# Kernel tuning notes

Measured on AMD Instinct MI355X. Metric: run time of the kernel, lower is better.

The kernel has to match this reference:

```python
import math
import jax, jax.numpy as jnp
import numpy as np

N_HEADS = 16

def setup_inputs() -> dict:
    key = jax.random.key(0)
    k1, k2, k3 = jax.random.split(key, 3)
    B, S, D = 2, 2048, 1024
    x = jax.random.normal(k1, (B, S, D), dtype=jnp.float32)
    W_qkv = jax.random.normal(k2, (3 * D, D), dtype=jnp.float32)
    W_o = jax.random.normal(k3, (D, D), dtype=jnp.float32)
    return {"x": x, "W_qkv": W_qkv, "W_o": W_o}


def reference(x, W_qkv, W_o):
    B, S, D = x.shape
    H = N_HEADS
    d_h = D // H
    # fused QKV projection: (B,S,3D)
    t = jnp.matmul(x, W_qkv.T)
    t = t.reshape(B, S, 3, D)
    # NOTE: module reshapes (B,S,D) -> (B,H,S,d_h) directly (no transpose);
    # heads partition the flattened seq*feature layout. Replicate exactly.
    q = t[:, :, 0, :].reshape(B, H, S, d_h)
    k = t[:, :, 1, :].reshape(B, H, S, d_h)
    v = t[:, :, 2, :].reshape(B, H, S, d_h)
    # scaled by sqrt(d_model), as in the original (not sqrt(d_h))
    scores = jnp.einsum('bhqd,bhkd->bhqk', q, k) / math.sqrt(D)
    scores = jnp.tril(scores)
    # original sets ALL exact zeros to -inf (masks upper triangle)
    scores = jnp.where(scores == 0, -jnp.inf, scores)
    attn = jax.nn.softmax(scores, axis=-1)
    y_prime = jnp.matmul(attn, v)  # (B,H,S,d_h)
    y_prime = y_prime.transpose(0, 2, 1, 3).reshape(B, S, D)
    y = jnp.matmul(y_prime, W_o.T)
    return y
```

## Files before the change

kernel.cpp:

```cpp
#include <hip/hip_runtime.h>
#include <hip/hip_bf16.h>


using bf16 = __hip_bfloat16;
typedef __attribute__((ext_vector_type(8))) short bf16x8v;
typedef __attribute__((ext_vector_type(4))) float f32x4;

#define MFMA_BF16(A, B, C) __builtin_amdgcn_mfma_f32_16x16x32_bf16((A), (B), (C), 0, 0, 0)

#define GLD_LDS16(g, l)                                                        \
  __builtin_amdgcn_global_load_lds(                                            \
      (const __attribute__((address_space(1))) void*)(g),                      \
      (__attribute__((address_space(3))) void*)(l), 16, 0, 0)

static __device__ __forceinline__ unsigned short bf_bits(float f) {
  bf16 b = __float2bfloat16(f);
  return *reinterpret_cast<unsigned short*>(&b);
}

__global__ __launch_bounds__(256) void cvt_split(const float* __restrict__ in,
                                                 bf16* __restrict__ hi,
                                                 bf16* __restrict__ lo, int n) {
  int i = (blockIdx.x * 256 + threadIdx.x) * 4;
  if (i >= n) return;
  const float4 v = *(const float4*)(in + i);
  float vv[4] = {v.x, v.y, v.z, v.w};
  ushort4 hb, lb;
  unsigned short* hp = &hb.x;
  unsigned short* lp = &lb.x;
#pragma unroll
  for (int j = 0; j < 4; ++j) {
    bf16 h = __float2bfloat16(vv[j]);
    float r = vv[j] - __bfloat162float(h);
    hp[j] = bf_bits(vv[j]);
    lp[j] = bf_bits(r);
  }
  *(ushort4*)(hi + i) = hb;
  *(ushort4*)(lo + i) = lb;
}

__global__ __launch_bounds__(256) void cvt_plain(const float* __restrict__ in,
                                                 bf16* __restrict__ out, int n) {
  int i = (blockIdx.x * 256 + threadIdx.x) * 4;
  if (i >= n) return;
  const float4 v = *(const float4*)(in + i);
  ushort4 ob;
  ob.x = bf_bits(v.x); ob.y = bf_bits(v.y); ob.z = bf_bits(v.z); ob.w = bf_bits(v.w);
  *(ushort4*)(out + i) = ob;
}

__global__ __launch_bounds__(256) void gemm_qkv(
    const bf16* __restrict__ Ah, const bf16* __restrict__ Al,
    const bf16* __restrict__ Bh, const bf16* __restrict__ Bl,
    bf16* __restrict__ Qhi, bf16* __restrict__ Qlo,
    bf16* __restrict__ Khi, bf16* __restrict__ Klo,
    bf16* __restrict__ Vt) {
  const int K = 1024;
  const int NT = 24;
  __shared__ __attribute__((aligned(16))) bf16 AsH[4096], AsL[4096], BsH[4096], BsL[4096];
  const int t = threadIdx.x;
  const int lane = t & 63;
  const int wave = t >> 6;
  const int wr = wave >> 1, wc = wave & 1;
  int bid = blockIdx.x;
  bid = (bid & 7) * (768 >> 3) + (bid >> 3);
  const int bm = bid / NT, bn = bid % NT;
  const int brow = bm * 128, bcol = bn * 128;
  const bool isV = (bcol >= 2048);
  const bf16* pAh = Ah + (size_t)brow * K;
  const bf16* pAl = Al + (size_t)brow * K;
  const bf16* pBh = Bh + (size_t)bcol * K;
  const bf16* pBl = Bl + (size_t)bcol * K;
  const int r0 = t >> 2;
  const int c0 = (t & 3) * 8;
  f32x4 acc[4][4] = {};
  for (int k0 = 0; k0 < K; k0 += 32) {
    __syncthreads();
    GLD_LDS16(pAh + (size_t)r0 * K + k0 + c0,        &AsH[t * 8]);
    GLD_LDS16(pAh + (size_t)(r0 + 64) * K + k0 + c0, &AsH[2048 + t * 8]);
    GLD_LDS16(pBh + (size_t)r0 * K + k0 + c0,        &BsH[t * 8]);
    GLD_LDS16(pBh + (size_t)(r0 + 64) * K + k0 + c0, &BsH[2048 + t * 8]);
    if (!isV) {
      GLD_LDS16(pAl + (size_t)r0 * K + k0 + c0,        &AsL[t * 8]);
      GLD_LDS16(pAl + (size_t)(r0 + 64) * K + k0 + c0, &AsL[2048 + t * 8]);
      GLD_LDS16(pBl + (size_t)r0 * K + k0 + c0,        &BsL[t * 8]);
      GLD_LDS16(pBl + (size_t)(r0 + 64) * K + k0 + c0, &BsL[2048 + t * 8]);
    }
    __syncthreads();
    const int ao = (wr * 64 + (lane & 15)) * 32 + (lane >> 4) * 8;
    const int bo = (wc * 64 + (lane & 15)) * 32 + (lane >> 4) * 8;
    bf16x8v ah[4], bh_[4];
#pragma unroll
    for (int i = 0; i < 4; ++i) {
      ah[i]  = *(const bf16x8v*)&AsH[ao + i * 512];
      bh_[i] = *(const bf16x8v*)&BsH[bo + i * 512];
    }
    if (!isV) {
      bf16x8v al[4], bl_[4];
#pragma unroll
      for (int i = 0; i < 4; ++i) {
        al[i]  = *(const bf16x8v*)&AsL[ao + i * 512];
        bl_[i] = *(const bf16x8v*)&BsL[bo + i * 512];
      }
#pragma unroll
      for (int i = 0; i < 4; ++i)
#pragma unroll
        for (int j = 0; j < 4; ++j) {
          acc[i][j] = MFMA_BF16(ah[i], bh_[j], acc[i][j]);
          acc[i][j] = MFMA_BF16(ah[i], bl_[j], acc[i][j]);
          acc[i][j] = MFMA_BF16(al[i], bh_[j], acc[i][j]);
        }
    } else {
#pragma unroll
      for (int i = 0; i < 4; ++i)
#pragma unroll
        for (int j = 0; j < 4; ++j)
          acc[i][j] = MFMA_BF16(ah[i], bh_[j], acc[i][j]);
    }
  }
#pragma unroll
  for (int i = 0; i < 4; ++i)
#pragma unroll
    for (int j = 0; j < 4; ++j)
#pragma unroll
      for (int e = 0; e < 4; ++e) {
        const int m = brow + wr * 64 + i * 16 + ((lane >> 4) << 2) + e;
        const int n = bcol + wc * 64 + j * 16 + (lane & 15);
        float v = acc[i][j][e];
        const int b = m >> 11, s = m & 2047;
        const int c = n >> 10, d = n & 1023;
        const int bh_i = (b << 4) | (s >> 7);
        const int s2 = ((s & 127) << 4) | (d >> 6);
        const int dh = d & 63;
        if (c == 2) {
          Vt[((size_t)bh_i << 17) | ((size_t)dh << 11) | (size_t)s2] = __float2bfloat16(v);
        } else {
          if (c == 0) v *= 0.03125f;
          const size_t idx = ((size_t)bh_i << 17) | ((size_t)s2 << 6) | (size_t)dh;
          bf16 hv = __float2bfloat16(v);
          bf16 lv = __float2bfloat16(v - __bfloat162float(hv));
          if (c == 0) { Qhi[idx] = hv; Qlo[idx] = lv; }
          else        { Khi[idx] = hv; Klo[idx] = lv; }
        }
      }
}

__global__ __launch_bounds__(64, 2) void attn_kernel(
    const bf16* __restrict__ Qhi, const bf16* __restrict__ Qlo,
    const bf16* __restrict__ Khi, const bf16* __restrict__ Klo,
    const bf16* __restrict__ Vt, bf16* __restrict__ Yp) {
  const int lane = threadIdx.x & 63;
  const int bh = blockIdx.x & 31;
  const int c  = 63 - (blockIdx.x >> 5);
  const int b = bh >> 4, h = bh & 15;
  const size_t base = (size_t)bh << 17;
  const bf16* qh_p = Qhi + base;
  const bf16* ql_p = Qlo + base;
  const bf16* kh_p = Khi + base;
  const bf16* kl_p = Klo + base;
  const bf16* v_p  = Vt + base;
  const int qbase = c << 5;
  const int l15 = lane & 15;
  const int lg  = lane >> 4;
  __shared__ __attribute__((aligned(16))) bf16 Plds[32][72];

  bf16x8v qfh[2][2], qfl[2][2];
#pragma unroll
  for (int q2 = 0; q2 < 2; ++q2)
#pragma unroll
    for (int x2 = 0; x2 < 2; ++x2) {
      const size_t o = (size_t)(qbase + q2 * 16 + l15) * 64 + x2 * 32 + lg * 8;
      qfh[q2][x2] = *(const bf16x8v*)(qh_p + o);
      qfl[q2][x2] = *(const bf16x8v*)(ql_p + o);
    }
  bf16x8v ones8;
#pragma unroll
  for (int j = 0; j < 8; ++j) ones8[j] = (short)0x3F80;

  f32x4 oac[2][4] = {};
  f32x4 oden[2] = {};
  float mrun[2] = {-3.0e38f, -3.0e38f};
  const float L2E = 1.4426950408889634f;
  const int nfull = c >> 1;

  bf16x8v kh0r[4], kh1r[4], kl0r[4], kl1r[4];
#define LOADK(kb_)                                                             \
  {                                                                            \
    const int _kb = (kb_);                                                     \
    _Pragma("unroll")                                                          \
    for (int kf = 0; kf < 4; ++kf) {                                           \
      const size_t ko = (size_t)(_kb + kf * 16 + l15) * 64 + lg * 8;           \
      kh0r[kf] = *(const bf16x8v*)(kh_p + ko);                                 \
      kh1r[kf] = *(const bf16x8v*)(kh_p + ko + 32);                            \
      kl0r[kf] = *(const bf16x8v*)(kl_p + ko);                                 \
      kl1r[kf] = *(const bf16x8v*)(kl_p + ko + 32);                            \
    }                                                                          \
  }
  LOADK(0);

  for (int kt = 0; kt <= nfull; ++kt) {
    const int kb = kt << 6;
    f32x4 st[4][2] = {};
#pragma unroll
    for (int kf = 0; kf < 4; ++kf)
#pragma unroll
      for (int q2 = 0; q2 < 2; ++q2) {
        f32x4 a = st[kf][q2];
        a = MFMA_BF16(kh0r[kf], qfh[q2][0], a);
        a = MFMA_BF16(kh1r[kf], qfh[q2][1], a);
        a = MFMA_BF16(kh0r[kf], qfl[q2][0], a);
        a = MFMA_BF16(kh1r[kf], qfl[q2][1], a);
        a = MFMA_BF16(kl0r[kf], qfh[q2][0], a);
        a = MFMA_BF16(kl1r[kf], qfh[q2][1], a);
        st[kf][q2] = a;
      }
    bf16x8v vreg[2][4];
#pragma unroll
    for (int x2 = 0; x2 < 2; ++x2)
#pragma unroll
      for (int df = 0; df < 4; ++df)
        vreg[x2][df] =
            *(const bf16x8v*)(v_p + (size_t)(df * 16 + l15) * 2048 + kb + x2 * 32 + lg * 8);
    if (kt < nfull) LOADK(kb + 64);
    if (kt == nfull) {
#pragma unroll
      for (int kf = 0; kf < 4; ++kf)
#pragma unroll
        for (int q2 = 0; q2 < 2; ++q2)
#pragma unroll
          for (int e = 0; e < 4; ++e) {
            const int key = kb + kf * 16 + (lg << 2) + e;
            const int qr  = qbase + q2 * 16 + l15;
            if (key > qr) st[kf][q2][e] = -3.0e38f;
          }
    }
    float tmax[2] = {-3.0e38f, -3.0e38f};
#pragma unroll
    for (int kf = 0; kf < 4; ++kf)
#pragma unroll
      for (int q2 = 0; q2 < 2; ++q2)
#pragma unroll
        for (int e = 0; e < 4; ++e)
          tmax[q2] = fmaxf(tmax[q2], st[kf][q2][e]);
#pragma unroll
    for (int q2 = 0; q2 < 2; ++q2) {
      tmax[q2] = fmaxf(tmax[q2], __shfl_xor(tmax[q2], 16));
      tmax[q2] = fmaxf(tmax[q2], __shfl_xor(tmax[q2], 32));
    }
    const int ok = (tmax[0] <= mrun[0] + 8.0f) && (tmax[1] <= mrun[1] + 8.0f);
    if (!__all(ok)) {
      float sfac[2];
#pragma unroll
      for (int q2 = 0; q2 < 2; ++q2) {
        const float mn = fmaxf(mrun[q2], tmax[q2]);
        sfac[q2] = exp2f((mrun[q2] - mn) * L2E);
        mrun[q2] = mn;
      }
#pragma unroll
      for (int q2 = 0; q2 < 2; ++q2)
#pragma unroll
        for (int e = 0; e < 4; ++e) {
          const float so = __shfl(sfac[q2], (lg << 2) + e);
          oden[q2][e] *= so;
#pragma unroll
          for (int df = 0; df < 4; ++df) oac[q2][df][e] *= so;
        }
    }
    const float mL0 = mrun[0] * L2E, mL1 = mrun[1] * L2E;
#pragma unroll
    for (int kf = 0; kf < 4; ++kf)
#pragma unroll
      for (int q2 = 0; q2 < 2; ++q2) {
        const float mL = q2 ? mL1 : mL0;
        ushort4 pk;
        unsigned short* pp = &pk.x;
#pragma unroll
        for (int e = 0; e < 4; ++e) {
          const float pv = exp2f(fmaf(st[kf][q2][e], L2E, -mL));
          pp[e] = bf_bits(pv);
        }
        *(ushort4*)&Plds[q2 * 16 + l15][kf * 16 + (lg << 2)] = pk;
      }
    asm volatile("s_waitcnt lgkmcnt(0)" ::: "memory");
    __builtin_amdgcn_sched_barrier(0);
    bf16x8v pa[2][2];
#pragma unroll
    for (int x2 = 0; x2 < 2; ++x2)
#pragma unroll
      for (int q2 = 0; q2 < 2; ++q2)
        pa[x2][q2] = *(const bf16x8v*)&Plds[q2 * 16 + l15][x2 * 32 + lg * 8];
    asm volatile("" ::: "memory");
#pragma unroll
    for (int x2 = 0; x2 < 2; ++x2) {
#pragma unroll
      for (int q2 = 0; q2 < 2; ++q2)
        oden[q2] = MFMA_BF16(pa[x2][q2], ones8, oden[q2]);
#pragma unroll
      for (int df = 0; df < 4; ++df)
#pragma unroll
        for (int q2 = 0; q2 < 2; ++q2)
          oac[q2][df] = MFMA_BF16(pa[x2][q2], vreg[x2][df], oac[q2][df]);
    }
  }
#undef LOADK
#pragma unroll
  for (int q2 = 0; q2 < 2; ++q2) {
    float li[4];
#pragma unroll
    for (int e = 0; e < 4; ++e) li[e] = 1.0f / oden[q2][e];
#pragma unroll
    for (int df = 0; df < 4; ++df)
#pragma unroll
      for (int e = 0; e < 4; ++e) {
        const int qr = qbase + q2 * 16 + (lg << 2) + e;
        const int dh = df * 16 + l15;
        Yp[(size_t)(b * 2048 + qr) * 1024 + h * 64 + dh] =
            __float2bfloat16(oac[q2][df][e] * li[e]);
      }
  }
}

__global__ __launch_bounds__(256) void gemm_out(const bf16* __restrict__ A,
                                                const bf16* __restrict__ B,
                                                float* __restrict__ C) {
  const int K = 1024;
  const int NT = 8;
  __shared__ __attribute__((aligned(16))) bf16 As[4096], Bs[4096];
  const int t = threadIdx.x;
  const int lane = t & 63;
  const int wave = t >> 6;
  const int wr = wave >> 1, wc = wave & 1;
  int bid = blockIdx.x;
  bid = (bid & 7) * (256 >> 3) + (bid >> 3);
  const int bm = bid / NT, bn = bid % NT;
  const int brow = bm * 128, bcol = bn * 128;
  const bf16* pA = A + (size_t)brow * K;
  const bf16* pB = B + (size_t)bcol * K;
  const int r0 = t >> 2;
  const int c0 = (t & 3) * 8;
  f32x4 acc[4][4] = {};
  for (int k0 = 0; k0 < K; k0 += 32) {
    __syncthreads();
    GLD_LDS16(pA + (size_t)r0 * K + k0 + c0,        &As[t * 8]);
    GLD_LDS16(pA + (size_t)(r0 + 64) * K + k0 + c0, &As[2048 + t * 8]);
    GLD_LDS16(pB + (size_t)r0 * K + k0 + c0,        &Bs[t * 8]);
    GLD_LDS16(pB + (size_t)(r0 + 64) * K + k0 + c0, &Bs[2048 + t * 8]);
    __syncthreads();
    bf16x8v af[4], bf_[4];
    const int ao = (wr * 64 + (lane & 15)) * 32 + (lane >> 4) * 8;
    const int bo = (wc * 64 + (lane & 15)) * 32 + (lane >> 4) * 8;
#pragma unroll
    for (int i = 0; i < 4; ++i) {
      af[i]  = *(const bf16x8v*)&As[ao + i * 512];
      bf_[i] = *(const bf16x8v*)&Bs[bo + i * 512];
    }
#pragma unroll
    for (int i = 0; i < 4; ++i)
#pragma unroll
      for (int j = 0; j < 4; ++j)
        acc[i][j] = MFMA_BF16(af[i], bf_[j], acc[i][j]);
  }
#pragma unroll
  for (int i = 0; i < 4; ++i)
#pragma unroll
    for (int j = 0; j < 4; ++j)
#pragma unroll
      for (int e = 0; e < 4; ++e) {
        const int m = brow + wr * 64 + i * 16 + ((lane >> 4) << 2) + e;
        const int n = bcol + wc * 64 + j * 16 + (lane & 15);
        C[(size_t)m * 1024 + n] = acc[i][j][e];
      }
}

extern "C" void kernel_launch(void* const* d_in, const int* in_sizes, int n_in,
                              void* d_out, int out_size, void* d_ws, size_t ws_size,
                              hipStream_t stream) {
  (void)in_sizes; (void)n_in; (void)out_size; (void)ws_size;
  const float* x    = (const float*)d_in[0];
  const float* wqkv = (const float*)d_in[1];
  const float* wo   = (const float*)d_in[2];
  float* out = (float*)d_out;

  const size_t NX = 4096ull * 1024;
  const size_t NW = 3072ull * 1024;
  const size_t NO = 1024ull * 1024;

  bf16* p = (bf16*)d_ws;
  bf16* xh  = p; p += NX;
  bf16* xl  = p; p += NX;
  bf16* wqh = p; p += NW;
  bf16* wql = p; p += NW;
  bf16* wob = p; p += NO;
  bf16* qhi = p; p += NX;
  bf16* qlo = p; p += NX;
  bf16* khi = p; p += NX;
  bf16* klo = p; p += NX;
  bf16* vt  = p; p += NX;
  bf16* yp  = p; p += NX;

  hipLaunchKernelGGL(cvt_split, dim3(NX / 1024), dim3(256), 0, stream, x, xh, xl, (int)NX);
  hipLaunchKernelGGL(cvt_split, dim3(NW / 1024), dim3(256), 0, stream, wqkv, wqh, wql, (int)NW);
  hipLaunchKernelGGL(cvt_plain, dim3(NO / 1024), dim3(256), 0, stream, wo, wob, (int)NO);
  hipLaunchKernelGGL(gemm_qkv, dim3(32 * 24), dim3(256), 0, stream,
                     xh, xl, wqh, wql, qhi, qlo, khi, klo, vt);
  hipLaunchKernelGGL(attn_kernel, dim3(2048), dim3(64), 0, stream,
                     qhi, qlo, khi, klo, vt, yp);
  hipLaunchKernelGGL(gemm_out, dim3(32 * 8), dim3(256), 0, stream, yp, wob, out);
}
```

Baseline: 320.3 us.

## Double-buffer QKV GEMM, split attention KV range across two waves, shrink out-GEMM tile

The QKV GEMM gains double-buffered LDS staging with explicit vmcnt waits, so the next K tile loads while the current one is computed. The attention kernel now runs two waves per block, each handling half of the key blocks, and merges their softmax max, denominator and output accumulators through shared memory. The old K register prefetch is dropped in favour of direct loads. The output GEMM uses 64x128 tiles, doubling the grid to raise occupancy. This adds LDS use and a cross-wave merge step in exchange for more parallelism and better load overlap.

```diff
diff --git a/kernel.cpp b/kernel.cpp
--- a/kernel.cpp
+++ b/kernel.cpp
@@ -57,7 +57,8 @@
     bf16* __restrict__ Vt) {
   const int K = 1024;
   const int NT = 24;
-  __shared__ __attribute__((aligned(16))) bf16 AsH[4096], AsL[4096], BsH[4096], BsL[4096];
+  __shared__ __attribute__((aligned(16))) bf16 AsH[2][4096], AsL[2][4096],
+                                               BsH[2][4096], BsL[2][4096];
   const int t = threadIdx.x;
   const int lane = t & 63;
   const int wave = t >> 6;
@@ -74,33 +75,49 @@
   const int r0 = t >> 2;
   const int c0 = (t & 3) * 8;
   f32x4 acc[4][4] = {};
-  for (int k0 = 0; k0 < K; k0 += 32) {
-    __syncthreads();
-    GLD_LDS16(pAh + (size_t)r0 * K + k0 + c0,        &AsH[t * 8]);
-    GLD_LDS16(pAh + (size_t)(r0 + 64) * K + k0 + c0, &AsH[2048 + t * 8]);
-    GLD_LDS16(pBh + (size_t)r0 * K + k0 + c0,        &BsH[t * 8]);
-    GLD_LDS16(pBh + (size_t)(r0 + 64) * K + k0 + c0, &BsH[2048 + t * 8]);
-    if (!isV) {
-      GLD_LDS16(pAl + (size_t)r0 * K + k0 + c0,        &AsL[t * 8]);
-      GLD_LDS16(pAl + (size_t)(r0 + 64) * K + k0 + c0, &AsL[2048 + t * 8]);
-      GLD_LDS16(pBl + (size_t)r0 * K + k0 + c0,        &BsL[t * 8]);
-      GLD_LDS16(pBl + (size_t)(r0 + 64) * K + k0 + c0, &BsL[2048 + t * 8]);
-    }
-    __syncthreads();
-    const int ao = (wr * 64 + (lane & 15)) * 32 + (lane >> 4) * 8;
-    const int bo = (wc * 64 + (lane & 15)) * 32 + (lane >> 4) * 8;
+
+#define STAGE(buf, k0_)                                                        \
+  {                                                                            \
+    const int _k = (k0_);                                                      \
+    GLD_LDS16(pAh + (size_t)r0 * K + _k + c0,        &AsH[buf][t * 8]);        \
+    GLD_LDS16(pAh + (size_t)(r0 + 64) * K + _k + c0, &AsH[buf][2048 + t * 8]); \
+    GLD_LDS16(pBh + (size_t)r0 * K + _k + c0,        &BsH[buf][t * 8]);        \
+    GLD_LDS16(pBh + (size_t)(r0 + 64) * K + _k + c0, &BsH[buf][2048 + t * 8]); \
+    if (!isV) {                                                                \
+      GLD_LDS16(pAl + (size_t)r0 * K + _k + c0,        &AsL[buf][t * 8]);      \
+      GLD_LDS16(pAl + (size_t)(r0 + 64) * K + _k + c0, &AsL[buf][2048 + t * 8]);\
+      GLD_LDS16(pBl + (size_t)r0 * K + _k + c0,        &BsL[buf][t * 8]);      \
+      GLD_LDS16(pBl + (size_t)(r0 + 64) * K + _k + c0, &BsL[buf][2048 + t * 8]);\
+    }                                                                          \
+  }
+
+  STAGE(0, 0);
+  const int ao = (wr * 64 + (lane & 15)) * 32 + (lane >> 4) * 8;
+  const int bo = (wc * 64 + (lane & 15)) * 32 + (lane >> 4) * 8;
+  for (int tk = 0; tk < 32; ++tk) {
+    const int cur = tk & 1;
+    if (tk < 31) {
+      STAGE(cur ^ 1, (tk + 1) * 32);
+      if (!isV) asm volatile("s_waitcnt vmcnt(8)" ::: "memory");
+      else      asm volatile("s_waitcnt vmcnt(4)" ::: "memory");
+    } else {
+      asm volatile("s_waitcnt vmcnt(0)" ::: "memory");
+    }
+    __builtin_amdgcn_sched_barrier(0);
+    __builtin_amdgcn_s_barrier();
+    asm volatile("" ::: "memory");
     bf16x8v ah[4], bh_[4];
 #pragma unroll
     for (int i = 0; i < 4; ++i) {
-      ah[i]  = *(const bf16x8v*)&AsH[ao + i * 512];
-      bh_[i] = *(const bf16x8v*)&BsH[bo + i * 512];
+      ah[i]  = *(const bf16x8v*)&AsH[cur][ao + i * 512];
+      bh_[i] = *(const bf16x8v*)&BsH[cur][bo + i * 512];
     }
     if (!isV) {
       bf16x8v al[4], bl_[4];
 #pragma unroll
       for (int i = 0; i < 4; ++i) {
-        al[i]  = *(const bf16x8v*)&AsL[ao + i * 512];
-        bl_[i] = *(const bf16x8v*)&BsL[bo + i * 512];
+        al[i]  = *(const bf16x8v*)&AsL[cur][ao + i * 512];
+        bl_[i] = *(const bf16x8v*)&BsL[cur][bo + i * 512];
       }
 #pragma unroll
       for (int i = 0; i < 4; ++i)
@@ -117,7 +134,12 @@
         for (int j = 0; j < 4; ++j)
           acc[i][j] = MFMA_BF16(ah[i], bh_[j], acc[i][j]);
     }
-  }
+    asm volatile("" ::: "memory");
+    __builtin_amdgcn_sched_barrier(0);
+    __builtin_amdgcn_s_barrier();
+    asm volatile("" ::: "memory");
+  }
+#undef STAGE
 #pragma unroll
   for (int i = 0; i < 4; ++i)
 #pragma unroll
@@ -145,11 +167,12 @@
       }
 }
 
-__global__ __launch_bounds__(64, 2) void attn_kernel(
+__global__ __launch_bounds__(128, 4) void attn_kernel(
     const bf16* __restrict__ Qhi, const bf16* __restrict__ Qlo,
     const bf16* __restrict__ Khi, const bf16* __restrict__ Klo,
     const bf16* __restrict__ Vt, bf16* __restrict__ Yp) {
   const int lane = threadIdx.x & 63;
+  const int wv   = threadIdx.x >> 6;
   const int bh = blockIdx.x & 31;
   const int c  = 63 - (blockIdx.x >> 5);
   const int b = bh >> 4, h = bh & 15;
@@ -162,7 +185,9 @@
   const int qbase = c << 5;
   const int l15 = lane & 15;
   const int lg  = lane >> 4;
-  __shared__ __attribute__((aligned(16))) bf16 Plds[32][72];
+
+  __shared__ __attribute__((aligned(16))) float Xch[64][44];
+  bf16* Plds = reinterpret_cast<bf16*>(&Xch[0][0]) + wv * 2304;
 
   bf16x8v qfh[2][2], qfl[2][2];
 #pragma unroll
@@ -181,48 +206,35 @@
   f32x4 oden[2] = {};
   float mrun[2] = {-3.0e38f, -3.0e38f};
   const float L2E = 1.4426950408889634f;
-  const int nfull = c >> 1;
-
-  bf16x8v kh0r[4], kh1r[4], kl0r[4], kl1r[4];
-#define LOADK(kb_)                                                             \
-  {                                                                            \
-    const int _kb = (kb_);                                                     \
-    _Pragma("unroll")                                                          \
-    for (int kf = 0; kf < 4; ++kf) {                                           \
-      const size_t ko = (size_t)(_kb + kf * 16 + l15) * 64 + lg * 8;           \
-      kh0r[kf] = *(const bf16x8v*)(kh_p + ko);                                 \
-      kh1r[kf] = *(const bf16x8v*)(kh_p + ko + 32);                            \
-      kl0r[kf] = *(const bf16x8v*)(kl_p + ko);                                 \
-      kl1r[kf] = *(const bf16x8v*)(kl_p + ko + 32);                            \
-    }                                                                          \
-  }
-  LOADK(0);
-
-  for (int kt = 0; kt <= nfull; ++kt) {
+  const int n  = (c >> 1) + 1;
+  const int h0 = (n + 1) >> 1;
+  const int kt0 = wv ? h0 : 0;
+  const int kt1 = wv ? n : h0;
+  const int diag = n - 1;
+
+  for (int kt = kt0; kt < kt1; ++kt) {
     const int kb = kt << 6;
     f32x4 st[4][2] = {};
 #pragma unroll
-    for (int kf = 0; kf < 4; ++kf)
+    for (int kf = 0; kf < 4; ++kf) {
+      const size_t ko = (size_t)(kb + kf * 16 + l15) * 64 + lg * 8;
+      const bf16x8v kh0 = *(const bf16x8v*)(kh_p + ko);
+      const bf16x8v kh1 = *(const bf16x8v*)(kh_p + ko + 32);
+      const bf16x8v kl0 = *(const bf16x8v*)(kl_p + ko);
+      const bf16x8v kl1 = *(const bf16x8v*)(kl_p + ko + 32);
 #pragma unroll
       for (int q2 = 0; q2 < 2; ++q2) {
         f32x4 a = st[kf][q2];
-        a = MFMA_BF16(kh0r[kf], qfh[q2][0], a);
-        a = MFMA_BF16(kh1r[kf], qfh[q2][1], a);
-        a = MFMA_BF16(kh0r[kf], qfl[q2][0], a);
-        a = MFMA_BF16(kh1r[kf], qfl[q2][1], a);
-        a = MFMA_BF16(kl0r[kf], qfh[q2][0], a);
-        a = MFMA_BF16(kl1r[kf], qfh[q2][1], a);
+        a = MFMA_BF16(kh0, qfh[q2][0], a);
+        a = MFMA_BF16(kh1, qfh[q2][1], a);
+        a = MFMA_BF16(kh0, qfl[q2][0], a);
+        a = MFMA_BF16(kh1, qfl[q2][1], a);
+        a = MFMA_BF16(kl0, qfh[q2][0], a);
+        a = MFMA_BF16(kl1, qfh[q2][1], a);
         st[kf][q2] = a;
       }
-    bf16x8v vreg[2][4];
-#pragma unroll
-    for (int x2 = 0; x2 < 2; ++x2)
-#pragma unroll
-      for (int df = 0; df < 4; ++df)
-        vreg[x2][df] =
-            *(const bf16x8v*)(v_p + (size_t)(df * 16 + l15) * 2048 + kb + x2 * 32 + lg * 8);
-    if (kt < nfull) LOADK(kb + 64);
-    if (kt == nfull) {
+    }
+    if (kt == diag) {
 #pragma unroll
       for (int kf = 0; kf < 4; ++kf)
 #pragma unroll
@@ -275,12 +287,17 @@
         ushort4 pk;
         unsigned short* pp = &pk.x;
 #pragma unroll
-        for (int e = 0; e < 4; ++e) {
-          const float pv = exp2f(fmaf(st[kf][q2][e], L2E, -mL));
-          pp[e] = bf_bits(pv);
-        }
-        *(ushort4*)&Plds[q2 * 16 + l15][kf * 16 + (lg << 2)] = pk;
-      }
+        for (int e = 0; e < 4; ++e)
+          pp[e] = bf_bits(exp2f(fmaf(st[kf][q2][e], L2E, -mL)));
+        *(ushort4*)(Plds + (q2 * 16 + l15) * 72 + kf * 16 + (lg << 2)) = pk;
+      }
+    bf16x8v vreg[2][4];
+#pragma unroll
+    for (int x2 = 0; x2 < 2; ++x2)
+#pragma unroll
+      for (int df = 0; df < 4; ++df)
+        vreg[x2][df] =
+            *(const bf16x8v*)(v_p + (size_t)(df * 16 + l15) * 2048 + kb + x2 * 32 + lg * 8);
     asm volatile("s_waitcnt lgkmcnt(0)" ::: "memory");
     __builtin_amdgcn_sched_barrier(0);
     bf16x8v pa[2][2];
@@ -288,7 +305,7 @@
     for (int x2 = 0; x2 < 2; ++x2)
 #pragma unroll
       for (int q2 = 0; q2 < 2; ++q2)
-        pa[x2][q2] = *(const bf16x8v*)&Plds[q2 * 16 + l15][x2 * 32 + lg * 8];
+        pa[x2][q2] = *(const bf16x8v*)(Plds + (q2 * 16 + l15) * 72 + x2 * 32 + lg * 8);
     asm volatile("" ::: "memory");
 #pragma unroll
     for (int x2 = 0; x2 < 2; ++x2) {
@@ -302,21 +319,58 @@
           oac[q2][df] = MFMA_BF16(pa[x2][q2], vreg[x2][df], oac[q2][df]);
     }
   }
-#undef LOADK
-#pragma unroll
-  for (int q2 = 0; q2 < 2; ++q2) {
-    float li[4];
-#pragma unroll
-    for (int e = 0; e < 4; ++e) li[e] = 1.0f / oden[q2][e];
-#pragma unroll
-    for (int df = 0; df < 4; ++df)
+
+  __syncthreads();
+  if (wv == 1) {
+    float* dst = &Xch[lane][0];
+    dst[0] = mrun[0];
+    dst[1] = mrun[1];
+#pragma unroll
+    for (int q2 = 0; q2 < 2; ++q2)
+#pragma unroll
+      for (int e = 0; e < 4; ++e) dst[2 + q2 * 4 + e] = oden[q2][e];
+#pragma unroll
+    for (int q2 = 0; q2 < 2; ++q2)
+#pragma unroll
+      for (int df = 0; df < 4; ++df)
+#pragma unroll
+        for (int e = 0; e < 4; ++e)
+          dst[10 + q2 * 16 + df * 4 + e] = oac[q2][df][e];
+  }
+  __syncthreads();
+  if (wv == 0) {
+    const float* src = &Xch[lane][0];
+#pragma unroll
+    for (int q2 = 0; q2 < 2; ++q2) {
+      const float m1 = src[q2];
+      const float mm = fmaxf(mrun[q2], m1);
+      const float f0c = exp2f((mrun[q2] - mm) * L2E);
+      const float f1c = exp2f((m1 - mm) * L2E);
 #pragma unroll
       for (int e = 0; e < 4; ++e) {
-        const int qr = qbase + q2 * 16 + (lg << 2) + e;
-        const int dh = df * 16 + l15;
-        Yp[(size_t)(b * 2048 + qr) * 1024 + h * 64 + dh] =
-            __float2bfloat16(oac[q2][df][e] * li[e]);
-      }
+        const float f0 = __shfl(f0c, (lg << 2) + e);
+        const float f1 = __shfl(f1c, (lg << 2) + e);
+        oden[q2][e] = oden[q2][e] * f0 + src[2 + q2 * 4 + e] * f1;
+#pragma unroll
+        for (int df = 0; df < 4; ++df)
+          oac[q2][df][e] = oac[q2][df][e] * f0 + src[10 + q2 * 16 + df * 4 + e] * f1;
+      }
+    }
+#pragma unroll
+    for (int q2 = 0; q2 < 2; ++q2) {
+      float li[4];
+#pragma unroll
+      for (int e = 0; e < 4; ++e) li[e] = 1.0f / oden[q2][e];
+#pragma unroll
+      for (int df = 0; df < 4; ++df)
+#pragma unroll
+        for (int e = 0; e < 4; ++e) {
+          const int qr = qbase + q2 * 16 + (lg << 2) + e;
+          const int dh = df * 16 + l15;
+          Yp[(size_t)(b * 2048 + qr) * 1024 + h * 64 + dh] =
+              __float2bfloat16(oac[q2][df][e] * li[e]);
+        }
+    }
   }
 }
 
@@ -325,48 +379,49 @@
                                                 float* __restrict__ C) {
   const int K = 1024;
   const int NT = 8;
-  __shared__ __attribute__((aligned(16))) bf16 As[4096], Bs[4096];
+  __shared__ __attribute__((aligned(16))) bf16 As[2048], Bs[4096];
   const int t = threadIdx.x;
   const int lane = t & 63;
   const int wave = t >> 6;
   const int wr = wave >> 1, wc = wave & 1;
   int bid = blockIdx.x;
-  bid = (bid & 7) * (256 >> 3) + (bid >> 3);
+  bid = (bid & 7) * (512 >> 3) + (bid >> 3);
   const int bm = bid / NT, bn = bid % NT;
-  const int brow = bm * 128, bcol = bn * 128;
+  const int brow = bm * 64, bcol = bn * 128;
   const bf16* pA = A + (size_t)brow * K;
   const bf16* pB = B + (size_t)bcol * K;
   const int r0 = t >> 2;
   const int c0 = (t & 3) * 8;
-  f32x4 acc[4][4] = {};
+  f32x4 acc[2][4] = {};
   for (int k0 = 0; k0 < K; k0 += 32) {
     __syncthreads();
     GLD_LDS16(pA + (size_t)r0 * K + k0 + c0,        &As[t * 8]);
-    GLD_LDS16(pA + (size_t)(r0 + 64) * K + k0 + c0, &As[2048 + t * 8]);
     GLD_LDS16(pB + (size_t)r0 * K + k0 + c0,        &Bs[t * 8]);
     GLD_LDS16(pB + (size_t)(r0 + 64) * K + k0 + c0, &Bs[2048 + t * 8]);
     __syncthreads();
-    bf16x8v af[4], bf_[4];
-    const int ao = (wr * 64 + (lane & 15)) * 32 + (lane >> 4) * 8;
-    const int bo = (wc * 64 + (lane & 15)) * 32 + (lane >> 4) * 8;
-#pragma unroll
-    for (int i = 0; i < 4; ++i) {
-      af[i]  = *(const bf16x8v*)&As[ao + i * 512];
-      bf_[i] = *(const bf16x8v*)&Bs[bo + i * 512];
-    }
-#pragma unroll
-    for (int i = 0; i < 4; ++i)
+    bf16x8v af[2], bf_[4];
+    const int l15 = lane & 15, lg = lane >> 4;
+#pragma unroll
+    for (int i = 0; i < 2; ++i)
+      af[i] = *(const bf16x8v*)&As[(wr * 32 + i * 16 + l15) * 32 + lg * 8];
+#pragma unroll
+    for (int j = 0; j < 4; ++j) {
+      const int rB = wc * 64 + j * 16 + l15;
+      bf_[j] = *(const bf16x8v*)&Bs[(rB & 63) * 32 + (rB >> 6) * 2048 + lg * 8];
+    }
+#pragma unroll
+    for (int i = 0; i < 2; ++i)
 #pragma unroll
       for (int j = 0; j < 4; ++j)
         acc[i][j] = MFMA_BF16(af[i], bf_[j], acc[i][j]);
   }
 #pragma unroll
-  for (int i = 0; i < 4; ++i)
+  for (int i = 0; i < 2; ++i)
 #pragma unroll
     for (int j = 0; j < 4; ++j)
 #pragma unroll
       for (int e = 0; e < 4; ++e) {
-        const int m = brow + wr * 64 + i * 16 + ((lane >> 4) << 2) + e;
+        const int m = brow + wr * 32 + i * 16 + ((lane >> 4) << 2) + e;
         const int n = bcol + wc * 64 + j * 16 + (lane & 15);
         C[(size_t)m * 1024 + n] = acc[i][j][e];
       }
@@ -403,7 +458,7 @@
   hipLaunchKernelGGL(cvt_plain, dim3(NO / 1024), dim3(256), 0, stream, wo, wob, (int)NO);
   hipLaunchKernelGGL(gemm_qkv, dim3(32 * 24), dim3(256), 0, stream,
                      xh, xl, wqh, wql, qhi, qlo, khi, klo, vt);
-  hipLaunchKernelGGL(attn_kernel, dim3(2048), dim3(64), 0, stream,
+  hipLaunchKernelGGL(attn_kernel, dim3(2048), dim3(128), 0, stream,
                      qhi, qlo, khi, klo, vt, yp);
-  hipLaunchKernelGGL(gemm_out, dim3(32 * 8), dim3(256), 0, stream, yp, wob, out);
-}
+  hipLaunchKernelGGL(gemm_out, dim3(64 * 8), dim3(256), 0, stream, yp, wob, out);
+}
```

Result: slower. 362.0 us (+13.0%).
